# Kernel optimization log

Hardware: AMD Instinct MI355X
Metric: run time of the kernel (lower is better)

Reference implementation:

```python
import jax, jax.numpy as jnp
import numpy as np
from jax import lax

D = 1024  # input_dim
H = 1024  # hidden_dim
N = 32
T = 512


def setup_inputs() -> dict:
    key = jax.random.key(0)
    k1, k2, k3, k4 = jax.random.split(key, 4)
    std = 1.0 / np.sqrt(D + H)
    x = jax.random.normal(k1, (N, T, D), dtype=jnp.float32)
    state = jax.random.normal(k2, (N, H), dtype=jnp.float32)
    weight = jax.random.normal(k3, (D + H, 3 * (D + H)), dtype=jnp.float32) * std
    bias = jax.random.normal(k4, (3 * (D + H),), dtype=jnp.float32) * std
    return {"x": x, "state": state, "weight": weight, "bias": bias}


def reference(x, state, weight, bias):
    # weight slices, matching get_weights()
    Wxt = weight[:D, : 3 * H]            # (D, 3H)
    Wxd = weight[:D, 3 * H :]            # (D, 3D)
    Whd = weight[D:, 3 * H :]            # (H, 3D)
    Whtg = weight[D:, : 2 * H]           # (H, 2H)
    Whtc = weight[D:, 2 * H : 3 * H]     # (H, H)

    # temporal pre-activations: (N, T, 3H)
    gates = jnp.einsum('ntd,dk->ntk', x, Wxt) + bias[: 3 * H]

    def step(prev_ht, g_t):
        # g_t: (N, 3H)
        gg = jax.nn.sigmoid(g_t[:, : 2 * H] + prev_ht @ Whtg)
        u = gg[:, :H]
        r = gg[:, H:]
        hc = jnp.tanh(g_t[:, 2 * H :] + (r * prev_ht) @ Whtc)
        ht = prev_ht + u * (hc - prev_ht)
        return ht, ht

    final_ht, ht_seq = lax.scan(step, state, jnp.swapaxes(gates, 0, 1))
    ht = jnp.swapaxes(ht_seq, 0, 1)  # (N, T, H)

    # depth gates: bias + ht @ Whd everywhere; +x @ Wxd only on gate part
    gd = jnp.einsum('nth,hk->ntk', ht, Whd) + bias[3 * H :]       # (N, T, 3D)
    g2 = jax.nn.sigmoid(gd[..., : 2 * D] + jnp.einsum('ntd,dk->ntk', x, Wxd[:, : 2 * D]))
    ud = g2[..., :D]
    rd = g2[..., D:]
    hcd = jnp.tanh(gd[..., 2 * D :] + jnp.einsum('ntd,dk->ntk', rd * x, Wxd[:, 2 * D :]))
    h = x + ud * (hcd - x)
    return h, final_ht
```

## Files before the change

### kernel.cpp

```cpp
#include <hip/hip_runtime.h>
#include <cstdint>
#include <cstddef>

typedef unsigned int uint;
typedef unsigned long long u64;
typedef __attribute__((ext_vector_type(8))) __bf16 bf16x8;
typedef __attribute__((ext_vector_type(4))) __bf16 bf16x4v;
typedef __attribute__((ext_vector_type(4))) float floatx4;

#define WLD 6144

static const size_t OFF_GATES = 0;
static const size_t OFF_XB    = 100663296;
static const size_t OFF_HTSEQ = 134217728;
static const size_t OFF_WHTGT = OFF_HTSEQ;
static const size_t OFF_WHTCT = OFF_HTSEQ + 4194304;
static const size_t OFF_WXTT  = 167772160;
static const size_t OFF_WHDT  = 174063616;
static const size_t OFF_WXD1T = 180355072;
static const size_t OFF_WXD2T = 184549376;
static const size_t OFF_HTG   = 186646528;
static const size_t OFF_RHG   = 186712064;
static const size_t OFF_BAR   = 186777600;

__device__ __forceinline__ float sigmoidf_(float x) { return 1.f / (1.f + __expf(-x)); }
__device__ __forceinline__ float tanhf_(float x) { float e = __expf(2.f * x); return 1.f - 2.f / (e + 1.f); }

__device__ __forceinline__ u64 ald(const __bf16* p) {
  return __hip_atomic_load((const u64*)p, __ATOMIC_RELAXED, __HIP_MEMORY_SCOPE_AGENT);
}
__device__ __forceinline__ void ast(__bf16* p, u64 v) {
  __hip_atomic_store((u64*)p, v, __ATOMIC_RELAXED, __HIP_MEMORY_SCOPE_AGENT);
}
union B8 { u64 u[2]; bf16x8 v; };


__global__ __launch_bounds__(256) void convert_x(const float4* __restrict__ x4,
                                                 __bf16* __restrict__ xb,
                                                 uint* __restrict__ bar) {
  if (blockIdx.x == 0) {
    __hip_atomic_store(bar + threadIdx.x, 0u, __ATOMIC_RELAXED, __HIP_MEMORY_SCOPE_AGENT);
    __hip_atomic_store(bar + 256 + threadIdx.x, 0u, __ATOMIC_RELAXED, __HIP_MEMORY_SCOPE_AGENT);
  }
  const int s = blockIdx.x;
  const int n = s >> 9, t = s & 511;
  const int d = (t << 5) | n;
  float4 v = x4[(size_t)s * 256 + threadIdx.x];
  bf16x4v o = { (__bf16)v.x, (__bf16)v.y, (__bf16)v.z, (__bf16)v.w };
  *reinterpret_cast<bf16x4v*>(xb + (size_t)d * 1024 + threadIdx.x * 4) = o;
}

__global__ __launch_bounds__(256) void transpose_conv(const float* __restrict__ src,
                                                      __bf16* __restrict__ dst) {
  __shared__ float t[32][33];
  const int ct = blockIdx.x, kt = blockIdx.y;
  const int j = threadIdx.x & 31, ig = threadIdx.x >> 5;
#pragma unroll
  for (int ii = 0; ii < 4; ++ii) {
    int i = ig * 4 + ii;
    t[i][j] = src[(size_t)(kt * 32 + i) * WLD + ct * 32 + j];
  }
  __syncthreads();
#pragma unroll
  for (int ii = 0; ii < 4; ++ii) {
    int cc = ig * 4 + ii;
    dst[(size_t)(ct * 32 + cc) * 1024 + kt * 32 + j] = (__bf16)t[j][cc];
  }
}

template <int MODE>
__global__ __launch_bounds__(256) void gemm_bt(const __bf16* __restrict__ A, int lda,
                                               const __bf16* __restrict__ BT,
                                               const float* __restrict__ bias,
                                               __bf16* __restrict__ gbuf,
                                               const float* __restrict__ xf,
                                               float* __restrict__ hout, int ncols) {
  __shared__ __bf16 As[128][48];
  __shared__ __bf16 Bs[128][48];
  const int tid = threadIdx.x;
  const int lane = tid & 63, wave = tid >> 6;
  const int tm = blockIdx.y, tn = blockIdx.x;
  const int wm = (wave & 1) * 64, wn = (wave >> 1) * 64;
  floatx4 acc[4][4] = {};
  const int c = tid & 3, r0 = tid >> 2;
  const size_t arow = (size_t)tm * 128;
  const size_t brow = (size_t)tn * 128;

  for (int kk = 0; kk < 1024; kk += 32) {
    *reinterpret_cast<uint4*>(&As[r0][c * 8]) =
        *reinterpret_cast<const uint4*>(A + (arow + r0) * (size_t)lda + kk + c * 8);
    *reinterpret_cast<uint4*>(&As[r0 + 64][c * 8]) =
        *reinterpret_cast<const uint4*>(A + (arow + r0 + 64) * (size_t)lda + kk + c * 8);
    *reinterpret_cast<uint4*>(&Bs[r0][c * 8]) =
        *reinterpret_cast<const uint4*>(BT + (brow + r0) * 1024 + kk + c * 8);
    *reinterpret_cast<uint4*>(&Bs[r0 + 64][c * 8]) =
        *reinterpret_cast<const uint4*>(BT + (brow + r0 + 64) * 1024 + kk + c * 8);
    __syncthreads();
    const int mr = lane & 15, kg = (lane >> 4) * 8;
    bf16x8 af[4], bfr[4];
#pragma unroll
    for (int f = 0; f < 4; ++f) af[f] = *reinterpret_cast<const bf16x8*>(&As[wm + f * 16 + mr][kg]);
#pragma unroll
    for (int f = 0; f < 4; ++f) bfr[f] = *reinterpret_cast<const bf16x8*>(&Bs[wn + f * 16 + mr][kg]);
#pragma unroll
    for (int fi = 0; fi < 4; ++fi)
#pragma unroll
      for (int fj = 0; fj < 4; ++fj)
        acc[fi][fj] = __builtin_amdgcn_mfma_f32_16x16x32_bf16(af[fi], bfr[fj], acc[fi][fj], 0, 0, 0);
    __syncthreads();
  }

#pragma unroll
  for (int fi = 0; fi < 4; ++fi)
#pragma unroll
    for (int fj = 0; fj < 4; ++fj) {
      const int row0 = tm * 128 + wm + fi * 16 + (lane >> 4) * 4;
      const int col = tn * 128 + wn + fj * 16 + (lane & 15);
#pragma unroll
      for (int r = 0; r < 4; ++r) {
        const size_t row = (size_t)(row0 + r);
        float v = acc[fi][fj][r];
        if (MODE == 0 || MODE == 1) {
          gbuf[row * 3072 + col] = (__bf16)(v + bias[col]);
        } else if (MODE == 2) {
          float g = sigmoidf_(v + (float)gbuf[row * 3072 + col]);
          const size_t xrow = (size_t)(row & 31) * 512 + (row >> 5);
          if (col < 1024)
            gbuf[row * 3072 + col] = (__bf16)g;
          else
            gbuf[row * 3072 + col] = (__bf16)(g * xf[xrow * 1024 + (col - 1024)]);
        } else {
          float hcd = tanhf_(v + (float)gbuf[row * 3072 + 2048 + col]);
          float ud = (float)gbuf[row * 3072 + col];
          const size_t xrow = (size_t)(row & 31) * 512 + (row >> 5);
          float xv = xf[xrow * 1024 + col];
          hout[xrow * 1024 + col] = xv + ud * (hcd - xv);
        }
      }
    }
}


__device__ __forceinline__ void gwait(uint* bar, uint e, volatile uint* lflag, int tid) {
  if (tid == 0) {
    while ((int)(__hip_atomic_load(bar, __ATOMIC_RELAXED, __HIP_MEMORY_SCOPE_AGENT) - 64u * e) < 0) {}
    lflag[0] = e;
  } else if ((tid & 63) == 0) {
    while ((int)(lflag[0] - e) < 0) {}
  }
}

#define SMEM_BYTES 138048
#define WS 1032
__global__ __launch_bounds__(512) void recur_kernel(
    const __bf16* __restrict__ gates, const float* __restrict__ state,
    const __bf16* __restrict__ whtg_t, const __bf16* __restrict__ whtc_t,
    __bf16* __restrict__ ht_g, __bf16* __restrict__ rh_g,
    __bf16* __restrict__ htseq, float* __restrict__ otail, uint* __restrict__ bar) {
  extern __shared__ char smem[];
  __bf16* Wg  = (__bf16*)smem;
  __bf16* Wc  = (__bf16*)(smem + 66048);
  float*  red = (float*)(smem + 99072);
  float*  u_s = (float*)(smem + 132864);
  float*  hp_s= (float*)(smem + 134912);
  __bf16* p_s = (__bf16*)(smem + 136960);
  volatile uint* lflag = (volatile uint*)(smem + 137984);

  const int b = blockIdx.x, tid = threadIdx.x;
  const int lane = tid & 63, w = tid >> 6;
  const int mr = lane & 15, kq = lane >> 4;
  const int k0 = w * 128;

  for (int idx = tid; idx < 4096; idx += 512) {
    int row = idx >> 7, seg = idx & 127;
    int src = (row < 16) ? (b * 16 + row) : (1024 + b * 16 + row - 16);
    *reinterpret_cast<uint4*>(Wg + row * WS + seg * 8) =
        *reinterpret_cast<const uint4*>(whtg_t + (size_t)src * 1024 + seg * 8);
  }
  for (int idx = tid; idx < 2048; idx += 512) {
    int row = idx >> 7, seg = idx & 127;
    *reinterpret_cast<uint4*>(Wc + row * WS + seg * 8) =
        *reinterpret_cast<const uint4*>(whtc_t + (size_t)(b * 16 + row) * 1024 + seg * 8);
  }
  {
    int n = tid >> 4, cc = tid & 15;
    float sv = state[n * 1024 + b * 16 + cc];
    hp_s[n * 16 + cc] = sv;
    p_s[n * 16 + cc] = (__bf16)sv;
    if (tid == 0) lflag[0] = 0;
  }
  __syncthreads();
  if (tid < 64) {
    u64* ps64 = (u64*)p_s;
    int i0 = tid, i1 = tid + 64;
    ast(ht_g + (i0 >> 2) * 1024 + b * 16 + (i0 & 3) * 4, ps64[i0]);
    ast(ht_g + (i1 >> 2) * 1024 + b * 16 + (i1 & 3) * 4, ps64[i1]);
    asm volatile("s_waitcnt vmcnt(0)" ::: "memory");
    if (tid == 0)
      (void)__hip_atomic_fetch_add(bar, 1u, __ATOMIC_RELAXED, __HIP_MEMORY_SCOPE_AGENT);
  }
  uint e = 1;

  for (int t = 0; t < 512; ++t) {
    {
      __bf16 graw0, graw1;
      {
        int n = tid >> 5, col = tid & 31;
        int cc = (col < 16) ? (b * 16 + col) : (1024 + b * 16 + col - 16);
        graw0 = gates[(size_t)(t * 32 + n) * 3072 + cc];
        int o2 = tid + 512, n2 = o2 >> 5, col2 = o2 & 31;
        int cc2 = (col2 < 16) ? (b * 16 + col2) : (1024 + b * 16 + col2 - 16);
        graw1 = gates[(size_t)(t * 32 + n2) * 3072 + cc2];
      }
      gwait(bar, e, lflag, tid);
      B8 a0[4], a1[4];
#pragma unroll
      for (int c2 = 0; c2 < 4; ++c2) {
        int kb = k0 + c2 * 32 + kq * 8;
        a0[c2].u[0] = ald(ht_g + mr * 1024 + kb);
        a0[c2].u[1] = ald(ht_g + mr * 1024 + kb + 4);
        a1[c2].u[0] = ald(ht_g + (16 + mr) * 1024 + kb);
        a1[c2].u[1] = ald(ht_g + (16 + mr) * 1024 + kb + 4);
      }
      floatx4 acc[2][2] = {};
#pragma unroll
      for (int c2 = 0; c2 < 4; ++c2) {
        int kb = k0 + c2 * 32 + kq * 8;
        bf16x8 b0 = *reinterpret_cast<const bf16x8*>(Wg + mr * WS + kb);
        bf16x8 b1 = *reinterpret_cast<const bf16x8*>(Wg + (16 + mr) * WS + kb);
        acc[0][0] = __builtin_amdgcn_mfma_f32_16x16x32_bf16(a0[c2].v, b0, acc[0][0], 0, 0, 0);
        acc[0][1] = __builtin_amdgcn_mfma_f32_16x16x32_bf16(a0[c2].v, b1, acc[0][1], 0, 0, 0);
        acc[1][0] = __builtin_amdgcn_mfma_f32_16x16x32_bf16(a1[c2].v, b0, acc[1][0], 0, 0, 0);
        acc[1][1] = __builtin_amdgcn_mfma_f32_16x16x32_bf16(a1[c2].v, b1, acc[1][1], 0, 0, 0);
      }
#pragma unroll
      for (int ai = 0; ai < 2; ++ai)
#pragma unroll
        for (int cj = 0; cj < 2; ++cj)
#pragma unroll
          for (int r = 0; r < 4; ++r)
            red[w * 1056 + (ai * 16 + kq * 4 + r) * 33 + cj * 16 + mr] = acc[ai][cj][r];
      __syncthreads();
      {
        int n = tid >> 5, col = tid & 31;
        float s = 0.f;
#pragma unroll
        for (int w8 = 0; w8 < 8; ++w8) s += red[w8 * 1056 + n * 33 + col];
        float gg = sigmoidf_(s + (float)graw0);
        if (col < 16) u_s[n * 16 + col] = gg;
        else p_s[n * 16 + (col - 16)] = (__bf16)(gg * hp_s[n * 16 + (col - 16)]);
        int o2 = tid + 512, n2 = o2 >> 5, col2 = o2 & 31;
        float s2 = 0.f;
#pragma unroll
        for (int w8 = 0; w8 < 8; ++w8) s2 += red[w8 * 1056 + n2 * 33 + col2];
        float gg2 = sigmoidf_(s2 + (float)graw1);
        if (col2 < 16) u_s[n2 * 16 + col2] = gg2;
        else p_s[n2 * 16 + (col2 - 16)] = (__bf16)(gg2 * hp_s[n2 * 16 + (col2 - 16)]);
      }
      __syncthreads();
      if (tid < 64) {
        u64* ps64 = (u64*)p_s;
        int i0 = tid, i1 = tid + 64;
        ast(rh_g + (i0 >> 2) * 1024 + b * 16 + (i0 & 3) * 4, ps64[i0]);
        ast(rh_g + (i1 >> 2) * 1024 + b * 16 + (i1 & 3) * 4, ps64[i1]);
        asm volatile("s_waitcnt vmcnt(0)" ::: "memory");
        if (tid == 0)
          (void)__hip_atomic_fetch_add(bar, 1u, __ATOMIC_RELAXED, __HIP_MEMORY_SCOPE_AGENT);
      }
    }
    {
      __bf16 gcraw;
      {
        int n = tid >> 4, col = tid & 15;
        gcraw = gates[(size_t)(t * 32 + n) * 3072 + 2048 + b * 16 + col];
      }
      gwait(bar, e + 1, lflag, tid);
      B8 a0[4], a1[4];
#pragma unroll
      for (int c2 = 0; c2 < 4; ++c2) {
        int kb = k0 + c2 * 32 + kq * 8;
        a0[c2].u[0] = ald(rh_g + mr * 1024 + kb);
        a0[c2].u[1] = ald(rh_g + mr * 1024 + kb + 4);
        a1[c2].u[0] = ald(rh_g + (16 + mr) * 1024 + kb);
        a1[c2].u[1] = ald(rh_g + (16 + mr) * 1024 + kb + 4);
      }
      floatx4 acc[2] = {};
#pragma unroll
      for (int c2 = 0; c2 < 4; ++c2) {
        int kb = k0 + c2 * 32 + kq * 8;
        bf16x8 bb = *reinterpret_cast<const bf16x8*>(Wc + mr * WS + kb);
        acc[0] = __builtin_amdgcn_mfma_f32_16x16x32_bf16(a0[c2].v, bb, acc[0], 0, 0, 0);
        acc[1] = __builtin_amdgcn_mfma_f32_16x16x32_bf16(a1[c2].v, bb, acc[1], 0, 0, 0);
      }
#pragma unroll
      for (int ai = 0; ai < 2; ++ai)
#pragma unroll
        for (int r = 0; r < 4; ++r)
          red[w * 1056 + (ai * 16 + kq * 4 + r) * 33 + mr] = acc[ai][r];
      __syncthreads();
      {
        int n = tid >> 4, col = tid & 15;
        float s = 0.f;
#pragma unroll
        for (int w8 = 0; w8 < 8; ++w8) s += red[w8 * 1056 + n * 33 + col];
        float hc = tanhf_(s + (float)gcraw);
        float hp = hp_s[n * 16 + col];
        float uu = u_s[n * 16 + col];
        float hn = hp + uu * (hc - hp);
        hp_s[n * 16 + col] = hn;
        p_s[n * 16 + col] = (__bf16)hn;
        htseq[(size_t)(t * 32 + n) * 1024 + b * 16 + col] = (__bf16)hn;
        if (t == 511) otail[n * 1024 + b * 16 + col] = hn;
      }
      __syncthreads();
      if (tid < 64) {
        u64* ps64 = (u64*)p_s;
        int i0 = tid, i1 = tid + 64;
        ast(ht_g + (i0 >> 2) * 1024 + b * 16 + (i0 & 3) * 4, ps64[i0]);
        ast(ht_g + (i1 >> 2) * 1024 + b * 16 + (i1 & 3) * 4, ps64[i1]);
        asm volatile("s_waitcnt vmcnt(0)" ::: "memory");
        if (tid == 0)
          (void)__hip_atomic_fetch_add(bar, 1u, __ATOMIC_RELAXED, __HIP_MEMORY_SCOPE_AGENT);
      }
    }
    e += 2;
  }
}


extern "C" void kernel_launch(void* const* d_in, const int* in_sizes, int n_in,
                              void* d_out, int out_size, void* d_ws, size_t ws_size,
                              hipStream_t stream) {
  const float* x = (const float*)d_in[0];
  const float* state = (const float*)d_in[1];
  const float* weight = (const float*)d_in[2];
  const float* bias = (const float*)d_in[3];
  float* out = (float*)d_out;
  char* ws = (char*)d_ws;

  __bf16* gates  = (__bf16*)(ws + OFF_GATES);
  __bf16* xb     = (__bf16*)(ws + OFF_XB);
  __bf16* htseq  = (__bf16*)(ws + OFF_HTSEQ);
  __bf16* whtg_t = (__bf16*)(ws + OFF_WHTGT);
  __bf16* whtc_t = (__bf16*)(ws + OFF_WHTCT);
  __bf16* wxtt   = (__bf16*)(ws + OFF_WXTT);
  __bf16* whdt   = (__bf16*)(ws + OFF_WHDT);
  __bf16* wxd1t  = (__bf16*)(ws + OFF_WXD1T);
  __bf16* wxd2t  = (__bf16*)(ws + OFF_WXD2T);
  __bf16* ht_g   = (__bf16*)(ws + OFF_HTG);
  __bf16* rh_g   = (__bf16*)(ws + OFF_RHG);
  uint*   bar    = (uint*)(ws + OFF_BAR);

  hipLaunchKernelGGL(convert_x, dim3(16384), dim3(256), 0, stream, (const float4*)x, xb, bar);
  hipLaunchKernelGGL(transpose_conv, dim3(96, 32), dim3(256), 0, stream, weight, wxtt);
  hipLaunchKernelGGL(transpose_conv, dim3(64, 32), dim3(256), 0, stream, weight + 3072, wxd1t);
  hipLaunchKernelGGL(transpose_conv, dim3(32, 32), dim3(256), 0, stream, weight + 5120, wxd2t);
  hipLaunchKernelGGL(transpose_conv, dim3(96, 32), dim3(256), 0, stream,
                     weight + (size_t)1024 * WLD + 3072, whdt);
  hipLaunchKernelGGL(transpose_conv, dim3(64, 32), dim3(256), 0, stream,
                     weight + (size_t)1024 * WLD, whtg_t);
  hipLaunchKernelGGL(transpose_conv, dim3(32, 32), dim3(256), 0, stream,
                     weight + (size_t)1024 * WLD + 2048, whtc_t);

  hipLaunchKernelGGL((gemm_bt<0>), dim3(24, 128), dim3(256), 0, stream,
                     xb, 1024, wxtt, bias, gates, (const float*)nullptr, (float*)nullptr, 3072);

  {
    (void)hipFuncSetAttribute(reinterpret_cast<const void*>(recur_kernel),
                              hipFuncAttributeMaxDynamicSharedMemorySize, SMEM_BYTES);
    const __bf16* gatesc = gates;
    float* otail = out + 16777216;
    void* args[9];
    args[0] = (void*)&gatesc; args[1] = (void*)&state;  args[2] = (void*)&whtg_t;
    args[3] = (void*)&whtc_t; args[4] = (void*)&ht_g;   args[5] = (void*)&rh_g;
    args[6] = (void*)&htseq;  args[7] = (void*)&otail;  args[8] = (void*)&bar;
    hipLaunchCooperativeKernel(recur_kernel, dim3(64), dim3(512), args, SMEM_BYTES, stream);
  }

  hipLaunchKernelGGL((gemm_bt<1>), dim3(24, 128), dim3(256), 0, stream,
                     htseq, 1024, whdt, bias + 3072, gates, (const float*)nullptr,
                     (float*)nullptr, 3072);
  hipLaunchKernelGGL((gemm_bt<2>), dim3(16, 128), dim3(256), 0, stream,
                     xb, 1024, wxd1t, bias, gates, x, (float*)nullptr, 2048);
  hipLaunchKernelGGL((gemm_bt<3>), dim3(8, 128), dim3(256), 0, stream,
                     gates + 1024, 3072, wxd2t, bias, gates, x, out, 1024);
}
```

Before: 7.114 ms.

## Replace global counter barrier with per-word epoch-tagged flags in recurrence

The recurrent kernel no longer uses a global atomic counter barrier plus a shared-memory relay. Each published pair of bf16 values is now packed into a 64-bit word together with its step epoch, and consumers spin until every word they read carries the expected tag. This removes the serialized fetch-add, the waitcnt drains and the extra syncthreads-then-store phase on the critical path of each half-step. In exchange it doubles the bytes read per hidden-state exchange, adds retry loops that re-read data, and needs a new kernel to zero the tags.

Measured after the change: 9.621 ms. 1.35x slower.

```diff
diff --git a/kernel.cpp b/kernel.cpp
--- a/kernel.cpp
+++ b/kernel.cpp
@@ -3,6 +3,7 @@
 #include <cstddef>
 
 typedef unsigned int uint;
+typedef unsigned short ushort;
 typedef unsigned long long u64;
 typedef __attribute__((ext_vector_type(8))) __bf16 bf16x8;
 typedef __attribute__((ext_vector_type(4))) __bf16 bf16x4v;
@@ -16,38 +17,38 @@
 static const size_t OFF_WHTGT = OFF_HTSEQ;
 static const size_t OFF_WHTCT = OFF_HTSEQ + 4194304;
 static const size_t OFF_WXTT  = 167772160;
+static const size_t OFF_TAGS  = OFF_WXTT;
 static const size_t OFF_WHDT  = 174063616;
 static const size_t OFF_WXD1T = 180355072;
 static const size_t OFF_WXD2T = 184549376;
-static const size_t OFF_HTG   = 186646528;
-static const size_t OFF_RHG   = 186712064;
-static const size_t OFF_BAR   = 186777600;
 
 __device__ __forceinline__ float sigmoidf_(float x) { return 1.f / (1.f + __expf(-x)); }
 __device__ __forceinline__ float tanhf_(float x) { float e = __expf(2.f * x); return 1.f - 2.f / (e + 1.f); }
 
-__device__ __forceinline__ u64 ald(const __bf16* p) {
-  return __hip_atomic_load((const u64*)p, __ATOMIC_RELAXED, __HIP_MEMORY_SCOPE_AGENT);
-}
-__device__ __forceinline__ void ast(__bf16* p, u64 v) {
-  __hip_atomic_store((u64*)p, v, __ATOMIC_RELAXED, __HIP_MEMORY_SCOPE_AGENT);
-}
-union B8 { u64 u[2]; bf16x8 v; };
+__device__ __forceinline__ u64 ald64(const u64* p) {
+  return __hip_atomic_load(p, __ATOMIC_RELAXED, __HIP_MEMORY_SCOPE_AGENT);
+}
+__device__ __forceinline__ void ast64(u64* p, u64 v) {
+  __hip_atomic_store(p, v, __ATOMIC_RELAXED, __HIP_MEMORY_SCOPE_AGENT);
+}
+__device__ __forceinline__ u64 mk_tag(uint e, float ve, float vo) {
+  union { __bf16 b; ushort u; } a, c; a.b = (__bf16)ve; c.b = (__bf16)vo;
+  return ((u64)e << 32) | ((u64)c.u << 16) | (u64)a.u;
+}
 
 
 __global__ __launch_bounds__(256) void convert_x(const float4* __restrict__ x4,
-                                                 __bf16* __restrict__ xb,
-                                                 uint* __restrict__ bar) {
-  if (blockIdx.x == 0) {
-    __hip_atomic_store(bar + threadIdx.x, 0u, __ATOMIC_RELAXED, __HIP_MEMORY_SCOPE_AGENT);
-    __hip_atomic_store(bar + 256 + threadIdx.x, 0u, __ATOMIC_RELAXED, __HIP_MEMORY_SCOPE_AGENT);
-  }
+                                                 __bf16* __restrict__ xb) {
   const int s = blockIdx.x;
   const int n = s >> 9, t = s & 511;
   const int d = (t << 5) | n;
   float4 v = x4[(size_t)s * 256 + threadIdx.x];
   bf16x4v o = { (__bf16)v.x, (__bf16)v.y, (__bf16)v.z, (__bf16)v.w };
   *reinterpret_cast<bf16x4v*>(xb + (size_t)d * 1024 + threadIdx.x * 4) = o;
+}
+
+__global__ __launch_bounds__(256) void zero_tags(u64* __restrict__ t) {
+  ast64(t + (size_t)blockIdx.x * 256 + threadIdx.x, 0ull);
 }
 
 __global__ __launch_bounds__(256) void transpose_conv(const float* __restrict__ src,
@@ -140,36 +141,25 @@
     }
 }
 
-
-__device__ __forceinline__ void gwait(uint* bar, uint e, volatile uint* lflag, int tid) {
-  if (tid == 0) {
-    while ((int)(__hip_atomic_load(bar, __ATOMIC_RELAXED, __HIP_MEMORY_SCOPE_AGENT) - 64u * e) < 0) {}
-    lflag[0] = e;
-  } else if ((tid & 63) == 0) {
-    while ((int)(lflag[0] - e) < 0) {}
-  }
-}
-
-#define SMEM_BYTES 138048
+#define SMEM_BYTES 136960
 #define WS 1032
 __global__ __launch_bounds__(512) void recur_kernel(
     const __bf16* __restrict__ gates, const float* __restrict__ state,
     const __bf16* __restrict__ whtg_t, const __bf16* __restrict__ whtc_t,
-    __bf16* __restrict__ ht_g, __bf16* __restrict__ rh_g,
-    __bf16* __restrict__ htseq, float* __restrict__ otail, uint* __restrict__ bar) {
+    u64* __restrict__ ht_w, u64* __restrict__ rh_w,
+    __bf16* __restrict__ htseq, float* __restrict__ otail) {
   extern __shared__ char smem[];
   __bf16* Wg  = (__bf16*)smem;
   __bf16* Wc  = (__bf16*)(smem + 66048);
   float*  red = (float*)(smem + 99072);
   float*  u_s = (float*)(smem + 132864);
   float*  hp_s= (float*)(smem + 134912);
-  __bf16* p_s = (__bf16*)(smem + 136960);
-  volatile uint* lflag = (volatile uint*)(smem + 137984);
 
   const int b = blockIdx.x, tid = threadIdx.x;
   const int lane = tid & 63, w = tid >> 6;
   const int mr = lane & 15, kq = lane >> 4;
   const int k0 = w * 128;
+  const int wbase = (k0 >> 1) + kq * 4;
 
   for (int idx = tid; idx < 4096; idx += 512) {
     int row = idx >> 7, seg = idx & 127;
@@ -186,22 +176,14 @@
     int n = tid >> 4, cc = tid & 15;
     float sv = state[n * 1024 + b * 16 + cc];
     hp_s[n * 16 + cc] = sv;
-    p_s[n * 16 + cc] = (__bf16)sv;
-    if (tid == 0) lflag[0] = 0;
+    float so = __shfl_xor(sv, 1);
+    if (!(cc & 1))
+      ast64(ht_w + (size_t)n * 512 + b * 8 + (cc >> 1), mk_tag(1u, sv, so));
   }
   __syncthreads();
-  if (tid < 64) {
-    u64* ps64 = (u64*)p_s;
-    int i0 = tid, i1 = tid + 64;
-    ast(ht_g + (i0 >> 2) * 1024 + b * 16 + (i0 & 3) * 4, ps64[i0]);
-    ast(ht_g + (i1 >> 2) * 1024 + b * 16 + (i1 & 3) * 4, ps64[i1]);
-    asm volatile("s_waitcnt vmcnt(0)" ::: "memory");
-    if (tid == 0)
-      (void)__hip_atomic_fetch_add(bar, 1u, __ATOMIC_RELAXED, __HIP_MEMORY_SCOPE_AGENT);
-  }
-  uint e = 1;
 
   for (int t = 0; t < 512; ++t) {
+    const uint e = (uint)t + 1u;
     {
       __bf16 graw0, graw1;
       {
@@ -212,26 +194,47 @@
         int cc2 = (col2 < 16) ? (b * 16 + col2) : (1024 + b * 16 + col2 - 16);
         graw1 = gates[(size_t)(t * 32 + n2) * 3072 + cc2];
       }
-      gwait(bar, e, lflag, tid);
-      B8 a0[4], a1[4];
+      {
+        bool rdy;
+        do {
+          u64 sgl = ald64(ht_w + (size_t)((w << 3) + (lane & 7)) * 8);
+          rdy = ((uint)(sgl >> 32) == e);
+        } while (!__all(rdy));
+      }
+      u64 wa[4][4], wb[4][4];
+      bool ok;
+      do {
+        ok = true;
+#pragma unroll
+        for (int c2 = 0; c2 < 4; ++c2) {
+          const size_t o0 = (size_t)mr * 512 + wbase + c2 * 16;
+          const size_t o1 = o0 + 16 * 512;
+#pragma unroll
+          for (int j = 0; j < 4; ++j) {
+            wa[c2][j] = ald64(ht_w + o0 + j);
+            wb[c2][j] = ald64(ht_w + o1 + j);
+          }
+        }
+#pragma unroll
+        for (int c2 = 0; c2 < 4; ++c2)
+#pragma unroll
+          for (int j = 0; j < 4; ++j)
+            ok = ok && ((uint)(wa[c2][j] >> 32) == e) && ((uint)(wb[c2][j] >> 32) == e);
+      } while (!__all(ok));
+
+      floatx4 acc[2][2] = {};
 #pragma unroll
       for (int c2 = 0; c2 < 4; ++c2) {
-        int kb = k0 + c2 * 32 + kq * 8;
-        a0[c2].u[0] = ald(ht_g + mr * 1024 + kb);
-        a0[c2].u[1] = ald(ht_g + mr * 1024 + kb + 4);
-        a1[c2].u[0] = ald(ht_g + (16 + mr) * 1024 + kb);
-        a1[c2].u[1] = ald(ht_g + (16 + mr) * 1024 + kb + 4);
-      }
-      floatx4 acc[2][2] = {};
-#pragma unroll
-      for (int c2 = 0; c2 < 4; ++c2) {
-        int kb = k0 + c2 * 32 + kq * 8;
+        union { uint4 u; bf16x8 v; } fa, fb;
+        fa.u = make_uint4((uint)wa[c2][0], (uint)wa[c2][1], (uint)wa[c2][2], (uint)wa[c2][3]);
+        fb.u = make_uint4((uint)wb[c2][0], (uint)wb[c2][1], (uint)wb[c2][2], (uint)wb[c2][3]);
+        const int kb = k0 + c2 * 32 + kq * 8;
         bf16x8 b0 = *reinterpret_cast<const bf16x8*>(Wg + mr * WS + kb);
         bf16x8 b1 = *reinterpret_cast<const bf16x8*>(Wg + (16 + mr) * WS + kb);
-        acc[0][0] = __builtin_amdgcn_mfma_f32_16x16x32_bf16(a0[c2].v, b0, acc[0][0], 0, 0, 0);
-        acc[0][1] = __builtin_amdgcn_mfma_f32_16x16x32_bf16(a0[c2].v, b1, acc[0][1], 0, 0, 0);
-        acc[1][0] = __builtin_amdgcn_mfma_f32_16x16x32_bf16(a1[c2].v, b0, acc[1][0], 0, 0, 0);
-        acc[1][1] = __builtin_amdgcn_mfma_f32_16x16x32_bf16(a1[c2].v, b1, acc[1][1], 0, 0, 0);
+        acc[0][0] = __builtin_amdgcn_mfma_f32_16x16x32_bf16(fa.v, b0, acc[0][0], 0, 0, 0);
+        acc[0][1] = __builtin_amdgcn_mfma_f32_16x16x32_bf16(fa.v, b1, acc[0][1], 0, 0, 0);
+        acc[1][0] = __builtin_amdgcn_mfma_f32_16x16x32_bf16(fb.v, b0, acc[1][0], 0, 0, 0);
+        acc[1][1] = __builtin_amdgcn_mfma_f32_16x16x32_bf16(fb.v, b1, acc[1][1], 0, 0, 0);
       }
 #pragma unroll
       for (int ai = 0; ai < 2; ++ai)
@@ -247,26 +250,25 @@
 #pragma unroll
         for (int w8 = 0; w8 < 8; ++w8) s += red[w8 * 1056 + n * 33 + col];
         float gg = sigmoidf_(s + (float)graw0);
+        float pub = 0.f;
         if (col < 16) u_s[n * 16 + col] = gg;
-        else p_s[n * 16 + (col - 16)] = (__bf16)(gg * hp_s[n * 16 + (col - 16)]);
+        else pub = gg * hp_s[n * 16 + (col - 16)];
+        float po = __shfl_xor(pub, 1);
+        if (col >= 16 && !(col & 1))
+          ast64(rh_w + (size_t)n * 512 + b * 8 + ((col - 16) >> 1), mk_tag(e, pub, po));
         int o2 = tid + 512, n2 = o2 >> 5, col2 = o2 & 31;
         float s2 = 0.f;
 #pragma unroll
         for (int w8 = 0; w8 < 8; ++w8) s2 += red[w8 * 1056 + n2 * 33 + col2];
         float gg2 = sigmoidf_(s2 + (float)graw1);
+        float pub2 = 0.f;
         if (col2 < 16) u_s[n2 * 16 + col2] = gg2;
-        else p_s[n2 * 16 + (col2 - 16)] = (__bf16)(gg2 * hp_s[n2 * 16 + (col2 - 16)]);
+        else pub2 = gg2 * hp_s[n2 * 16 + (col2 - 16)];
+        float po2 = __shfl_xor(pub2, 1);
+        if (col2 >= 16 && !(col2 & 1))
+          ast64(rh_w + (size_t)n2 * 512 + b * 8 + ((col2 - 16) >> 1), mk_tag(e, pub2, po2));
       }
       __syncthreads();
-      if (tid < 64) {
-        u64* ps64 = (u64*)p_s;
-        int i0 = tid, i1 = tid + 64;
-        ast(rh_g + (i0 >> 2) * 1024 + b * 16 + (i0 & 3) * 4, ps64[i0]);
-        ast(rh_g + (i1 >> 2) * 1024 + b * 16 + (i1 & 3) * 4, ps64[i1]);
-        asm volatile("s_waitcnt vmcnt(0)" ::: "memory");
-        if (tid == 0)
-          (void)__hip_atomic_fetch_add(bar, 1u, __ATOMIC_RELAXED, __HIP_MEMORY_SCOPE_AGENT);
-      }
     }
     {
       __bf16 gcraw;
@@ -274,23 +276,44 @@
         int n = tid >> 4, col = tid & 15;
         gcraw = gates[(size_t)(t * 32 + n) * 3072 + 2048 + b * 16 + col];
       }
-      gwait(bar, e + 1, lflag, tid);
-      B8 a0[4], a1[4];
+      {
+        bool rdy;
+        do {
+          u64 sgl = ald64(rh_w + (size_t)((w << 3) + (lane & 7)) * 8);
+          rdy = ((uint)(sgl >> 32) == e);
+        } while (!__all(rdy));
+      }
+      u64 wa[4][4], wb[4][4];
+      bool ok;
+      do {
+        ok = true;
+#pragma unroll
+        for (int c2 = 0; c2 < 4; ++c2) {
+          const size_t o0 = (size_t)mr * 512 + wbase + c2 * 16;
+          const size_t o1 = o0 + 16 * 512;
+#pragma unroll
+          for (int j = 0; j < 4; ++j) {
+            wa[c2][j] = ald64(rh_w + o0 + j);
+            wb[c2][j] = ald64(rh_w + o1 + j);
+          }
+        }
+#pragma unroll
+        for (int c2 = 0; c2 < 4; ++c2)
+#pragma unroll
+          for (int j = 0; j < 4; ++j)
+            ok = ok && ((uint)(wa[c2][j] >> 32) == e) && ((uint)(wb[c2][j] >> 32) == e);
+      } while (!__all(ok));
+
+      floatx4 acc[2] = {};
 #pragma unroll
       for (int c2 = 0; c2 < 4; ++c2) {
-        int kb = k0 + c2 * 32 + kq * 8;
-        a0[c2].u[0] = ald(rh_g + mr * 1024 + kb);
-        a0[c2].u[1] = ald(rh_g + mr * 1024 + kb + 4);
-        a1[c2].u[0] = ald(rh_g + (16 + mr) * 1024 + kb);
-        a1[c2].u[1] = ald(rh_g + (16 + mr) * 1024 + kb + 4);
-      }
-      floatx4 acc[2] = {};
-#pragma unroll
-      for (int c2 = 0; c2 < 4; ++c2) {
-        int kb = k0 + c2 * 32 + kq * 8;
+        union { uint4 u; bf16x8 v; } fa, fb;
+        fa.u = make_uint4((uint)wa[c2][0], (uint)wa[c2][1], (uint)wa[c2][2], (uint)wa[c2][3]);
+        fb.u = make_uint4((uint)wb[c2][0], (uint)wb[c2][1], (uint)wb[c2][2], (uint)wb[c2][3]);
+        const int kb = k0 + c2 * 32 + kq * 8;
         bf16x8 bb = *reinterpret_cast<const bf16x8*>(Wc + mr * WS + kb);
-        acc[0] = __builtin_amdgcn_mfma_f32_16x16x32_bf16(a0[c2].v, bb, acc[0], 0, 0, 0);
-        acc[1] = __builtin_amdgcn_mfma_f32_16x16x32_bf16(a1[c2].v, bb, acc[1], 0, 0, 0);
+        acc[0] = __builtin_amdgcn_mfma_f32_16x16x32_bf16(fa.v, bb, acc[0], 0, 0, 0);
+        acc[1] = __builtin_amdgcn_mfma_f32_16x16x32_bf16(fb.v, bb, acc[1], 0, 0, 0);
       }
 #pragma unroll
       for (int ai = 0; ai < 2; ++ai)
@@ -308,22 +331,14 @@
         float uu = u_s[n * 16 + col];
         float hn = hp + uu * (hc - hp);
         hp_s[n * 16 + col] = hn;
-        p_s[n * 16 + col] = (__bf16)hn;
         htseq[(size_t)(t * 32 + n) * 1024 + b * 16 + col] = (__bf16)hn;
         if (t == 511) otail[n * 1024 + b * 16 + col] = hn;
+        float ho = __shfl_xor(hn, 1);
+        if (!(col & 1))
+          ast64(ht_w + (size_t)n * 512 + b * 8 + (col >> 1), mk_tag(e + 1u, hn, ho));
       }
       __syncthreads();
-      if (tid < 64) {
-        u64* ps64 = (u64*)p_s;
-        int i0 = tid, i1 = tid + 64;
-        ast(ht_g + (i0 >> 2) * 1024 + b * 16 + (i0 & 3) * 4, ps64[i0]);
-        ast(ht_g + (i1 >> 2) * 1024 + b * 16 + (i1 & 3) * 4, ps64[i1]);
-        asm volatile("s_waitcnt vmcnt(0)" ::: "memory");
-        if (tid == 0)
-          (void)__hip_atomic_fetch_add(bar, 1u, __ATOMIC_RELAXED, __HIP_MEMORY_SCOPE_AGENT);
-      }
     }
-    e += 2;
   }
 }
 
@@ -347,11 +362,11 @@
   __bf16* whdt   = (__bf16*)(ws + OFF_WHDT);
   __bf16* wxd1t  = (__bf16*)(ws + OFF_WXD1T);
   __bf16* wxd2t  = (__bf16*)(ws + OFF_WXD2T);
-  __bf16* ht_g   = (__bf16*)(ws + OFF_HTG);
-  __bf16* rh_g   = (__bf16*)(ws + OFF_RHG);
-  uint*   bar    = (uint*)(ws + OFF_BAR);
-
-  hipLaunchKernelGGL(convert_x, dim3(16384), dim3(256), 0, stream, (const float4*)x, xb, bar);
+  u64*    tags   = (u64*)(ws + OFF_TAGS);
+  u64*    ht_w   = tags;
+  u64*    rh_w   = tags + 16384;
+
+  hipLaunchKernelGGL(convert_x, dim3(16384), dim3(256), 0, stream, (const float4*)x, xb);
   hipLaunchKernelGGL(transpose_conv, dim3(96, 32), dim3(256), 0, stream, weight, wxtt);
   hipLaunchKernelGGL(transpose_conv, dim3(64, 32), dim3(256), 0, stream, weight + 3072, wxd1t);
   hipLaunchKernelGGL(transpose_conv, dim3(32, 32), dim3(256), 0, stream, weight + 5120, wxd2t);
@@ -365,15 +380,17 @@
   hipLaunchKernelGGL((gemm_bt<0>), dim3(24, 128), dim3(256), 0, stream,
                      xb, 1024, wxtt, bias, gates, (const float*)nullptr, (float*)nullptr, 3072);
 
+  hipLaunchKernelGGL(zero_tags, dim3(128), dim3(256), 0, stream, tags);
+
   {
     (void)hipFuncSetAttribute(reinterpret_cast<const void*>(recur_kernel),
                               hipFuncAttributeMaxDynamicSharedMemorySize, SMEM_BYTES);
     const __bf16* gatesc = gates;
     float* otail = out + 16777216;
-    void* args[9];
+    void* args[8];
     args[0] = (void*)&gatesc; args[1] = (void*)&state;  args[2] = (void*)&whtg_t;
-    args[3] = (void*)&whtc_t; args[4] = (void*)&ht_g;   args[5] = (void*)&rh_g;
-    args[6] = (void*)&htseq;  args[7] = (void*)&otail;  args[8] = (void*)&bar;
+    args[3] = (void*)&whtc_t; args[4] = (void*)&ht_w;   args[5] = (void*)&rh_w;
+    args[6] = (void*)&htseq;  args[7] = (void*)&otail;
     hipLaunchCooperativeKernel(recur_kernel, dim3(64), dim3(512), args, SMEM_BYTES, stream);
   }
 
```
